# Optimization experiments

Measured on AMD Instinct MI355X. Metric: run time of the kernel, lower is better.

## Reference

```python
import jax, jax.numpy as jnp
import numpy as np

EPS = 1.0  # epsilon: defaults to 1.0 for scale-invariant kernels (thin_plate_spline)
TPS_MIN = 1e-7  # clamp in thin_plate_spline
NX, N, NDIM, M = 32768, 4096, 3, 16


def monomial_powers(ndim, degree):
    # replicates RBFBlock.monomial_powers for ndim=3, degree=1
    from itertools import combinations_with_replacement
    import math
    nmonos = math.comb(degree + ndim, ndim)
    out = np.zeros((nmonos, ndim), dtype=np.int32)
    count = 0
    for deg in range(degree + 1):
        for mono in combinations_with_replacement(range(ndim), deg):
            for var in mono:
                out[count, var] += 1
            count += 1
    return out


def setup_inputs() -> dict:
    key = jax.random.key(0)
    k1, k2, k3, k4 = jax.random.split(key, 4)
    powers = jnp.asarray(monomial_powers(NDIM, 1))  # (4, 3)
    return {
        "x": jax.random.normal(k1, (NX, NDIM), dtype=jnp.float32),
        "y": jax.random.normal(k2, (N, NDIM), dtype=jnp.float32),
        "shift": jax.random.normal(k3, (NDIM,), dtype=jnp.float32),
        "scale": jnp.ones((NDIM,), dtype=jnp.float32),
        "coeffs": jax.random.normal(k4, (N + powers.shape[0], M), dtype=jnp.float32) * 0.05,
        "powers": powers,
    }


def _cdist(a, b):
    # Euclidean distance matrix (na, nb) via the matmul identity; avoids (na, nb, d) blowup.
    a2 = jnp.sum(a * a, axis=1, keepdims=True)       # (na, 1)
    b2 = jnp.sum(b * b, axis=1, keepdims=True).T     # (1, nb)
    sq = a2 + b2 - 2.0 * (a @ b.T)
    return jnp.sqrt(jnp.maximum(sq, 0.0))


def _thin_plate_spline(r):
    r = jnp.maximum(r, TPS_MIN)
    return r * r * jnp.log(r)


def reference(x, y, shift, scale, coeffs, powers):
    # kernel part: phi(||eps*x - eps*y||)
    kv = _thin_plate_spline(_cdist(x * EPS, y * EPS))          # (nx, n)
    # polynomial part on normalized coords
    xhat = (x - shift) / scale                                  # (nx, d)
    p = jnp.prod(xhat[:, None, :] ** powers[None, :, :].astype(x.dtype), axis=-1)  # (nx, r)
    vec = jnp.concatenate([kv, p], axis=1)                      # (nx, n+r)
    return vec @ coeffs                                         # (nx, m)
```

## Files before the change

kernel.cpp:

```cpp
#include <hip/hip_runtime.h>

#define NXROWS 32768
#define NY     4096
#define MCOLS  16
#define BLOCK  256
#define KSPLIT 8
#define KCHUNK (NY / KSPLIT)
#define NITER  (KCHUNK / 32)
#define ROWS_PER_BLOCK 256
#define GRIDX  (NXROWS / ROWS_PER_BLOCK)

#define TPS_C 0.34657359027997264f

typedef __bf16 bf16x8 __attribute__((ext_vector_type(8)));
typedef short  s16x8  __attribute__((ext_vector_type(8)));
typedef float  f32x4  __attribute__((ext_vector_type(4)));

#define WS_Y4_OFF   0
#define WS_CT_OFF   65536
#define WS_PART_OFF 262144
#define WS_END      (WS_PART_OFF + (size_t)KSPLIT * NXROWS * MCOLS * 4)

static __device__ __forceinline__ unsigned short f2bfu(float f) {
    __bf16 h = (__bf16)f;
    return __builtin_bit_cast(unsigned short, h);
}

__global__ __launch_bounds__(BLOCK) void rbf_prep3(
    const float* __restrict__ y, const float* __restrict__ coeffs,
    float4* __restrict__ y4, unsigned int* __restrict__ cTw)
{
    const int idx = blockIdx.x * BLOCK + threadIdx.x;
    if (idx < MCOLS * NY / 2) {
        const int m  = idx >> 11;
        const int jp = (idx & 2047) * 2;
        const unsigned short u0 = f2bfu(TPS_C * coeffs[(size_t)jp * MCOLS + m]);
        const unsigned short u1 = f2bfu(TPS_C * coeffs[(size_t)(jp + 1) * MCOLS + m]);
        cTw[((size_t)m * NY + jp) >> 1] = (unsigned int)u0 | ((unsigned int)u1 << 16);
    } else {
        const int j = idx - MCOLS * NY / 2;
        const float y0 = y[3 * j], y1 = y[3 * j + 1], y2 = y[3 * j + 2];
        y4[j] = make_float4(y0, y1, y2, y0 * y0 + y1 * y1 + y2 * y2);
    }
}

__global__ __launch_bounds__(BLOCK, 4) void rbf_mfma4(
    const float* __restrict__ x, const float4* __restrict__ y4,
    const unsigned short* __restrict__ cT, float* __restrict__ part)
{
    const int lane = threadIdx.x & 63;
    const int wid  = threadIdx.x >> 6;
    const int n    = lane & 15;
    const int q    = lane >> 4;
    const int rowBase = blockIdx.x * ROWS_PER_BLOCK + wid * 64;
    const int kbase = blockIdx.y * KCHUNK;

    float sx[4], a0[4], a1[4], a2[4];
    #pragma unroll
    for (int t = 0; t < 4; ++t) {
        const int r = rowBase + t * 16 + n;
        const float c0 = x[r * 3], c1 = x[r * 3 + 1], c2 = x[r * 3 + 2];
        sx[t] = c0 * c0 + c1 * c1 + c2 * c2;
        a0[t] = -2.f * c0; a1[t] = -2.f * c1; a2[t] = -2.f * c2;
    }

    const float4* yb = y4 + kbase + q * 8;
    const unsigned short* cb = cT + (size_t)n * NY + kbase + q * 8;

    f32x4 acc[4];
    #pragma unroll
    for (int t = 0; t < 4; ++t) acc[t] = (f32x4){0.f, 0.f, 0.f, 0.f};

    for (int ks = 0; ks < NITER; ++ks) {
        float4 yv[8];
        #pragma unroll
        for (int e = 0; e < 8; ++e) yv[e] = yb[ks * 32 + e];
        const s16x8 braw = *reinterpret_cast<const s16x8*>(cb + ks * 32);

        bf16x8 af[4];
        #pragma unroll
        for (int e = 0; e < 8; ++e) {
            const float4 v = yv[e];
            #pragma unroll
            for (int t = 0; t < 4; ++t) {
                float s = fmaf(a0[t], v.x,
                          fmaf(a1[t], v.y,
                          fmaf(a2[t], v.z, sx[t] + v.w)));
                s = fmaxf(s, 1e-14f);
                af[t][e] = (__bf16)(s * __log2f(s));
            }
        }
        const bf16x8 bf = __builtin_bit_cast(bf16x8, braw);
        #pragma unroll
        for (int t = 0; t < 4; ++t)
            acc[t] = __builtin_amdgcn_mfma_f32_16x16x32_bf16(af[t], bf, acc[t], 0, 0, 0);
    }

    float* plane = part + (size_t)blockIdx.y * NXROWS * MCOLS;
    #pragma unroll
    for (int t = 0; t < 4; ++t) {
        float* o = plane + (size_t)(rowBase + t * 16 + q * 4) * MCOLS + n;
        #pragma unroll
        for (int r = 0; r < 4; ++r) o[(size_t)r * MCOLS] = acc[t][r];
    }
}

__global__ __launch_bounds__(BLOCK) void rbf_reduce(
    const float* __restrict__ part, const float* __restrict__ x,
    const float* __restrict__ shift, const float* __restrict__ scale,
    const float* __restrict__ coeffs, const int* __restrict__ powers,
    int nR, float* __restrict__ out)
{
    const int idx = blockIdx.x * BLOCK + threadIdx.x;
    const int row = idx >> 2, mq = idx & 3;
    f32x4 s = {0.f, 0.f, 0.f, 0.f};
    #pragma unroll
    for (int sp = 0; sp < KSPLIT; ++sp) {
        const f32x4 v = *reinterpret_cast<const f32x4*>(
            part + (size_t)sp * NXROWS * MCOLS + (size_t)row * MCOLS + mq * 4);
        s += v;
    }
    float xh[3];
    #pragma unroll
    for (int d = 0; d < 3; ++d) xh[d] = (x[row * 3 + d] - shift[d]) / scale[d];
    for (int r = 0; r < nR; ++r) {
        float p = 1.0f;
        for (int d = 0; d < 3; ++d) {
            const int pw = powers[r * 3 + d];
            for (int k = 0; k < pw; ++k) p *= xh[d];
        }
        const f32x4 cv = *reinterpret_cast<const f32x4*>(
            coeffs + (size_t)(NY + r) * MCOLS + mq * 4);
        s += p * cv;
    }
    *reinterpret_cast<f32x4*>(out + (size_t)row * MCOLS + mq * 4) = s;
}

__global__ __launch_bounds__(BLOCK) void rbf_f32_atomic(
    const float* __restrict__ x, const float* __restrict__ y,
    const float* __restrict__ coeffs, float* __restrict__ out)
{
    const int jbase = blockIdx.y * 512;
    const int row = blockIdx.x * BLOCK + threadIdx.x;
    const float x0 = x[row * 3], x1 = x[row * 3 + 1], x2 = x[row * 3 + 2];
    float acc[MCOLS];
    #pragma unroll
    for (int m = 0; m < MCOLS; ++m) acc[m] = 0.f;
    const float4* c4 = reinterpret_cast<const float4*>(coeffs) + (size_t)jbase * 4;
    for (int j = 0; j < 512; ++j) {
        const float dx = x0 - y[(jbase + j) * 3 + 0];
        const float dy = x1 - y[(jbase + j) * 3 + 1];
        const float dz = x2 - y[(jbase + j) * 3 + 2];
        const float sq = fmaxf(dx * dx + dy * dy + dz * dz, 1e-14f);
        const float t = TPS_C * sq * __log2f(sq);
        #pragma unroll
        for (int g = 0; g < 4; ++g) {
            const float4 cv = c4[j * 4 + g];
            acc[g * 4 + 0] += t * cv.x; acc[g * 4 + 1] += t * cv.y;
            acc[g * 4 + 2] += t * cv.z; acc[g * 4 + 3] += t * cv.w;
        }
    }
    #pragma unroll
    for (int m = 0; m < MCOLS; ++m)
        atomicAdd(&out[(size_t)row * MCOLS + m], acc[m]);
}

__global__ __launch_bounds__(BLOCK) void rbf_poly_atomic(
    const float* __restrict__ x, const float* __restrict__ shift,
    const float* __restrict__ scale, const float* __restrict__ coeffs,
    const int* __restrict__ powers, int nR, float* __restrict__ out)
{
    const int idx = blockIdx.x * BLOCK + threadIdx.x;
    const int row = idx >> 2, mq = idx & 3;
    float xh[3];
    #pragma unroll
    for (int d = 0; d < 3; ++d) xh[d] = (x[row * 3 + d] - shift[d]) / scale[d];
    f32x4 s = {0.f, 0.f, 0.f, 0.f};
    for (int r = 0; r < nR; ++r) {
        float p = 1.0f;
        for (int d = 0; d < 3; ++d) {
            const int pw = powers[r * 3 + d];
            for (int k = 0; k < pw; ++k) p *= xh[d];
        }
        const f32x4 cv = *reinterpret_cast<const f32x4*>(
            coeffs + (size_t)(NY + r) * MCOLS + mq * 4);
        s += p * cv;
    }
    float* o = out + (size_t)row * MCOLS + mq * 4;
    atomicAdd(o + 0, s.x); atomicAdd(o + 1, s.y);
    atomicAdd(o + 2, s.z); atomicAdd(o + 3, s.w);
}

extern "C" void kernel_launch(void* const* d_in, const int* in_sizes, int n_in,
                              void* d_out, int out_size, void* d_ws, size_t ws_size,
                              hipStream_t stream) {
    const float* x      = (const float*)d_in[0];
    const float* y      = (const float*)d_in[1];
    const float* shift  = (const float*)d_in[2];
    const float* scale  = (const float*)d_in[3];
    const float* coeffs = (const float*)d_in[4];
    const int*   powers = (const int*)d_in[5];
    const int    nR     = in_sizes[5] / 3;
    float* out = (float*)d_out;

    if (ws_size >= WS_END) {
        char* ws = (char*)d_ws;
        float4*         y4   = (float4*)(ws + WS_Y4_OFF);
        unsigned short* cT   = (unsigned short*)(ws + WS_CT_OFF);
        unsigned int*   cTw  = (unsigned int*)(ws + WS_CT_OFF);
        float*          part = (float*)(ws + WS_PART_OFF);
        rbf_prep3<<<(MCOLS * NY / 2 + NY) / BLOCK, BLOCK, 0, stream>>>(
            y, coeffs, y4, cTw);
        rbf_mfma4<<<dim3(GRIDX, KSPLIT), BLOCK, 0, stream>>>(x, y4, cT, part);
        rbf_reduce<<<NXROWS * 4 / BLOCK, BLOCK, 0, stream>>>(
            part, x, shift, scale, coeffs, powers, nR, out);
    } else {
        hipMemsetAsync(d_out, 0, (size_t)out_size * sizeof(float), stream);
        rbf_f32_atomic<<<dim3(NXROWS / BLOCK, NY / 512), BLOCK, 0, stream>>>(
            x, y, coeffs, out);
        rbf_poly_atomic<<<NXROWS * 4 / BLOCK, BLOCK, 0, stream>>>(
            x, shift, scale, coeffs, powers, nR, out);
    }
}
```

Measured before the change: 110.6 us.

## Stage y and coefficient chunks in LDS and double the K split

The MFMA kernel now loads its K-chunk of y (with the -2 factor folded into y during prep) and the bf16 coefficients into padded shared memory once per block, and reads from LDS inside the loop instead of global memory. KSPLIT goes from 8 to 16 so each block's chunk (256 entries) fits a single cooperative load, and occupancy is raised to 8 blocks per CU. The partial buffer and the reduce pass double in size, and each block now waits on a barrier after its load.

Result: slower. 118.5 us (+7.1%).

```diff
diff --git a/kernel.cpp b/kernel.cpp
--- a/kernel.cpp
+++ b/kernel.cpp
@@ -4,7 +4,7 @@
 #define NY     4096
 #define MCOLS  16
 #define BLOCK  256
-#define KSPLIT 8
+#define KSPLIT 16
 #define KCHUNK (NY / KSPLIT)
 #define NITER  (KCHUNK / 32)
 #define ROWS_PER_BLOCK 256
@@ -40,20 +40,38 @@
     } else {
         const int j = idx - MCOLS * NY / 2;
         const float y0 = y[3 * j], y1 = y[3 * j + 1], y2 = y[3 * j + 2];
-        y4[j] = make_float4(y0, y1, y2, y0 * y0 + y1 * y1 + y2 * y2);
-    }
-}
-
-__global__ __launch_bounds__(BLOCK, 4) void rbf_mfma4(
+        y4[j] = make_float4(-2.f * y0, -2.f * y1, -2.f * y2,
+                            y0 * y0 + y1 * y1 + y2 * y2);
+    }
+}
+
+__global__ __launch_bounds__(BLOCK, 8) void rbf_mfma5(
     const float* __restrict__ x, const float4* __restrict__ y4,
-    const unsigned short* __restrict__ cT, float* __restrict__ part)
-{
-    const int lane = threadIdx.x & 63;
-    const int wid  = threadIdx.x >> 6;
+    const unsigned int* __restrict__ cTw, float* __restrict__ part)
+{
+    __shared__ float4 ys[KCHUNK + KCHUNK / 8];
+    __shared__ unsigned short cs[MCOLS][KCHUNK + 8];
+
+    const int tid   = threadIdx.x;
+    const int kbase = blockIdx.y * KCHUNK;
+
+    ys[tid + (tid >> 3)] = y4[kbase + tid];
+    {
+        unsigned int* csw = reinterpret_cast<unsigned int*>(&cs[0][0]);
+        #pragma unroll
+        for (int i = tid; i < MCOLS * KCHUNK / 2; i += BLOCK) {
+            const int m = i >> 7;
+            const int c = i & 127;
+            csw[m * ((KCHUNK + 8) / 2) + c] = cTw[m * (NY / 2) + kbase / 2 + c];
+        }
+    }
+    __syncthreads();
+
+    const int lane = tid & 63;
+    const int wid  = tid >> 6;
     const int n    = lane & 15;
     const int q    = lane >> 4;
     const int rowBase = blockIdx.x * ROWS_PER_BLOCK + wid * 64;
-    const int kbase = blockIdx.y * KCHUNK;
 
     float sx[4], a0[4], a1[4], a2[4];
     #pragma unroll
@@ -61,26 +79,22 @@
         const int r = rowBase + t * 16 + n;
         const float c0 = x[r * 3], c1 = x[r * 3 + 1], c2 = x[r * 3 + 2];
         sx[t] = c0 * c0 + c1 * c1 + c2 * c2;
-        a0[t] = -2.f * c0; a1[t] = -2.f * c1; a2[t] = -2.f * c2;
-    }
-
-    const float4* yb = y4 + kbase + q * 8;
-    const unsigned short* cb = cT + (size_t)n * NY + kbase + q * 8;
+        a0[t] = c0; a1[t] = c1; a2[t] = c2;
+    }
+
+    const float4* ysp = ys + q * 9;
+    const unsigned short* csp = &cs[n][q * 8];
 
     f32x4 acc[4];
     #pragma unroll
     for (int t = 0; t < 4; ++t) acc[t] = (f32x4){0.f, 0.f, 0.f, 0.f};
 
     for (int ks = 0; ks < NITER; ++ks) {
-        float4 yv[8];
-        #pragma unroll
-        for (int e = 0; e < 8; ++e) yv[e] = yb[ks * 32 + e];
-        const s16x8 braw = *reinterpret_cast<const s16x8*>(cb + ks * 32);
-
+        const s16x8 braw = *reinterpret_cast<const s16x8*>(csp + ks * 32);
         bf16x8 af[4];
         #pragma unroll
         for (int e = 0; e < 8; ++e) {
-            const float4 v = yv[e];
+            const float4 v = ysp[ks * 36 + e];
             #pragma unroll
             for (int t = 0; t < 4; ++t) {
                 float s = fmaf(a0[t], v.x,
@@ -205,13 +219,12 @@
 
     if (ws_size >= WS_END) {
         char* ws = (char*)d_ws;
-        float4*         y4   = (float4*)(ws + WS_Y4_OFF);
-        unsigned short* cT   = (unsigned short*)(ws + WS_CT_OFF);
-        unsigned int*   cTw  = (unsigned int*)(ws + WS_CT_OFF);
-        float*          part = (float*)(ws + WS_PART_OFF);
+        float4*       y4   = (float4*)(ws + WS_Y4_OFF);
+        unsigned int* cTw  = (unsigned int*)(ws + WS_CT_OFF);
+        float*        part = (float*)(ws + WS_PART_OFF);
         rbf_prep3<<<(MCOLS * NY / 2 + NY) / BLOCK, BLOCK, 0, stream>>>(
             y, coeffs, y4, cTw);
-        rbf_mfma4<<<dim3(GRIDX, KSPLIT), BLOCK, 0, stream>>>(x, y4, cT, part);
+        rbf_mfma5<<<dim3(GRIDX, KSPLIT), BLOCK, 0, stream>>>(x, y4, cTw, part);
         rbf_reduce<<<NXROWS * 4 / BLOCK, BLOCK, 0, stream>>>(
             part, x, shift, scale, coeffs, powers, nR, out);
     } else {
```

## Compute squared distances with split-bf16 MFMA and permute into the coefficient MFMA

Applied to the files above, without the earlier changes.

The per-pair squared-distance FMAs are replaced by an MFMA. x and y are encoded as bf16 hi/lo splits so that a 16x16x32 bf16 MFMA yields |x|^2+|y|^2-2x·y in fp32. The distance tiles are then transformed by s*log2(s), packed to bf16, and rearranged across lanes with ds_bpermute into the A-operand layout for the existing coefficient MFMA. This moves most of the VALU distance arithmetic onto matrix cores, at the cost of extra MFMAs, cross-lane permutes, and some accuracy loss from the hi/lo bf16 splitting.

Result: slower. 116.3 us (+5.1%).

```diff
diff --git a/kernel.cpp b/kernel.cpp
--- a/kernel.cpp
+++ b/kernel.cpp
@@ -15,8 +15,9 @@
 typedef __bf16 bf16x8 __attribute__((ext_vector_type(8)));
 typedef short  s16x8  __attribute__((ext_vector_type(8)));
 typedef float  f32x4  __attribute__((ext_vector_type(4)));
-
-#define WS_Y4_OFF   0
+typedef unsigned int u32x4 __attribute__((ext_vector_type(4)));
+
+#define WS_Y8_OFF   0
 #define WS_CT_OFF   65536
 #define WS_PART_OFF 262144
 #define WS_END      (WS_PART_OFF + (size_t)KSPLIT * NXROWS * MCOLS * 4)
@@ -25,10 +26,13 @@
     __bf16 h = (__bf16)f;
     return __builtin_bit_cast(unsigned short, h);
 }
-
-__global__ __launch_bounds__(BLOCK) void rbf_prep3(
+static __device__ __forceinline__ unsigned int pku(float a, float b) {
+    return (unsigned int)f2bfu(a) | ((unsigned int)f2bfu(b) << 16);
+}
+
+__global__ __launch_bounds__(BLOCK) void rbf_prep4(
     const float* __restrict__ y, const float* __restrict__ coeffs,
-    float4* __restrict__ y4, unsigned int* __restrict__ cTw)
+    u32x4* __restrict__ y8, unsigned int* __restrict__ cTw)
 {
     const int idx = blockIdx.x * BLOCK + threadIdx.x;
     if (idx < MCOLS * NY / 2) {
@@ -40,31 +44,55 @@
     } else {
         const int j = idx - MCOLS * NY / 2;
         const float y0 = y[3 * j], y1 = y[3 * j + 1], y2 = y[3 * j + 2];
-        y4[j] = make_float4(y0, y1, y2, y0 * y0 + y1 * y1 + y2 * y2);
-    }
-}
-
-__global__ __launch_bounds__(BLOCK, 4) void rbf_mfma4(
-    const float* __restrict__ x, const float4* __restrict__ y4,
+        const float m0 = -2.f * y0, m1 = -2.f * y1, m2 = -2.f * y2;
+        const float s  = y0 * y0 + y1 * y1 + y2 * y2;
+        const float h0 = (float)(__bf16)m0, h1 = (float)(__bf16)m1, h2 = (float)(__bf16)m2;
+        const float sh = (float)(__bf16)s;
+        u32x4 v;
+        v.x = pku(h0, h1);
+        v.y = pku(h2, m0 - h0);
+        v.z = pku(m1 - h1, m2 - h2);
+        v.w = pku(s, s - sh);
+        y8[j] = v;
+    }
+}
+
+__global__ __launch_bounds__(BLOCK, 4) void rbf_mfma8(
+    const float* __restrict__ x, const u32x4* __restrict__ y8,
     const unsigned short* __restrict__ cT, float* __restrict__ part)
 {
     const int lane = threadIdx.x & 63;
     const int wid  = threadIdx.x >> 6;
     const int n    = lane & 15;
     const int q    = lane >> 4;
+    const bool q0  = (q == 0), q1 = (q == 1), q01 = (q < 2);
     const int rowBase = blockIdx.x * ROWS_PER_BLOCK + wid * 64;
     const int kbase = blockIdx.y * KCHUNK;
 
-    float sx[4], a0[4], a1[4], a2[4];
+    s16x8 bx[4];
     #pragma unroll
     for (int t = 0; t < 4; ++t) {
         const int r = rowBase + t * 16 + n;
-        const float c0 = x[r * 3], c1 = x[r * 3 + 1], c2 = x[r * 3 + 2];
-        sx[t] = c0 * c0 + c1 * c1 + c2 * c2;
-        a0[t] = -2.f * c0; a1[t] = -2.f * c1; a2[t] = -2.f * c2;
-    }
-
-    const float4* yb = y4 + kbase + q * 8;
+        const float x0 = x[r * 3], x1 = x[r * 3 + 1], x2 = x[r * 3 + 2];
+        const float s  = x0 * x0 + x1 * x1 + x2 * x2;
+        const float h0 = (float)(__bf16)x0, h1 = (float)(__bf16)x1, h2 = (float)(__bf16)x2;
+        const float sh = (float)(__bf16)s;
+        const unsigned int a0 = pku(h0, h1), a1 = pku(h2, h0), a2 = pku(h1, h2);
+        const unsigned int a3 = 0x3F803F80u;
+        const unsigned int b0 = pku(x0 - h0, x1 - h1);
+        const unsigned int b1 = pku(x2 - h2, s);
+        const unsigned int b2 = pku(s - sh, 0.f);
+        u32x4 w;
+        w.x = q0 ? a0 : (q1 ? b0 : 0u);
+        w.y = q0 ? a1 : (q1 ? b1 : 0u);
+        w.z = q0 ? a2 : (q1 ? b2 : 0u);
+        w.w = q0 ? a3 : 0u;
+        bx[t] = __builtin_bit_cast(s16x8, w);
+    }
+
+    const int ad1 = 4 * (n + 16 * ((2 * q) & 3));
+    const int ad2 = 4 * (n + 16 * ((2 * q + 1) & 3));
+
     const unsigned short* cb = cT + (size_t)n * NY + kbase + q * 8;
 
     f32x4 acc[4];
@@ -72,28 +100,60 @@
     for (int t = 0; t < 4; ++t) acc[t] = (f32x4){0.f, 0.f, 0.f, 0.f};
 
     for (int ks = 0; ks < NITER; ++ks) {
-        float4 yv[8];
+        const u32x4 Ylo = y8[kbase + ks * 32 + n];
+        const u32x4 Yhi = y8[kbase + ks * 32 + 16 + n];
+        const s16x8 bc  = *reinterpret_cast<const s16x8*>(cb + ks * 32);
+
+        u32x4 wa, wb;
+        wa.x = q01 ? Ylo.x : 0u;
+        wa.y = q0 ? Ylo.y : (q1 ? ((Ylo.y & 0xFFFFu) | 0x3F800000u) : 0u);
+        wa.z = q0 ? Ylo.z : (q1 ? 0x00003F80u : 0u);
+        wa.w = q0 ? Ylo.w : 0u;
+        wb.x = q01 ? Yhi.x : 0u;
+        wb.y = q0 ? Yhi.y : (q1 ? ((Yhi.y & 0xFFFFu) | 0x3F800000u) : 0u);
+        wb.z = q0 ? Yhi.z : (q1 ? 0x00003F80u : 0u);
+        wb.w = q0 ? Yhi.w : 0u;
+        const bf16x8 Alo = __builtin_bit_cast(bf16x8, wa);
+        const bf16x8 Ahi = __builtin_bit_cast(bf16x8, wb);
+        const bf16x8 bcf = __builtin_bit_cast(bf16x8, bc);
+
         #pragma unroll
-        for (int e = 0; e < 8; ++e) yv[e] = yb[ks * 32 + e];
-        const s16x8 braw = *reinterpret_cast<const s16x8*>(cb + ks * 32);
-
-        bf16x8 af[4];
-        #pragma unroll
-        for (int e = 0; e < 8; ++e) {
-            const float4 v = yv[e];
+        for (int t = 0; t < 4; ++t) {
+            const bf16x8 bxt = __builtin_bit_cast(bf16x8, bx[t]);
+            f32x4 Dlo = __builtin_amdgcn_mfma_f32_16x16x32_bf16(
+                Alo, bxt, (f32x4){0.f, 0.f, 0.f, 0.f}, 0, 0, 0);
+            f32x4 Dhi = __builtin_amdgcn_mfma_f32_16x16x32_bf16(
+                Ahi, bxt, (f32x4){0.f, 0.f, 0.f, 0.f}, 0, 0, 0);
+            float tl[4], th[4];
             #pragma unroll
-            for (int t = 0; t < 4; ++t) {
-                float s = fmaf(a0[t], v.x,
-                          fmaf(a1[t], v.y,
-                          fmaf(a2[t], v.z, sx[t] + v.w)));
-                s = fmaxf(s, 1e-14f);
-                af[t][e] = (__bf16)(s * __log2f(s));
+            for (int r = 0; r < 4; ++r) {
+                float sl = fmaxf(Dlo[r], 1e-14f);
+                float sh = fmaxf(Dhi[r], 1e-14f);
+                tl[r] = sl * __log2f(sl);
+                th[r] = sh * __log2f(sh);
             }
-        }
-        const bf16x8 bf = __builtin_bit_cast(bf16x8, braw);
-        #pragma unroll
-        for (int t = 0; t < 4; ++t)
-            acc[t] = __builtin_amdgcn_mfma_f32_16x16x32_bf16(af[t], bf, acc[t], 0, 0, 0);
+            const int ul0 = (int)pku(tl[0], tl[1]);
+            const int ul1 = (int)pku(tl[2], tl[3]);
+            const int uh0 = (int)pku(th[0], th[1]);
+            const int uh1 = (int)pku(th[2], th[3]);
+            u32x4 wp;
+            {
+                const int l0 = __builtin_amdgcn_ds_bpermute(ad1, ul0);
+                const int h0 = __builtin_amdgcn_ds_bpermute(ad1, uh0);
+                const int l1 = __builtin_amdgcn_ds_bpermute(ad1, ul1);
+                const int h1 = __builtin_amdgcn_ds_bpermute(ad1, uh1);
+                const int l2 = __builtin_amdgcn_ds_bpermute(ad2, ul0);
+                const int h2 = __builtin_amdgcn_ds_bpermute(ad2, uh0);
+                const int l3 = __builtin_amdgcn_ds_bpermute(ad2, ul1);
+                const int h3 = __builtin_amdgcn_ds_bpermute(ad2, uh1);
+                wp.x = (unsigned int)(q01 ? l0 : h0);
+                wp.y = (unsigned int)(q01 ? l1 : h1);
+                wp.z = (unsigned int)(q01 ? l2 : h2);
+                wp.w = (unsigned int)(q01 ? l3 : h3);
+            }
+            const bf16x8 A2 = __builtin_bit_cast(bf16x8, wp);
+            acc[t] = __builtin_amdgcn_mfma_f32_16x16x32_bf16(A2, bcf, acc[t], 0, 0, 0);
+        }
     }
 
     float* plane = part + (size_t)blockIdx.y * NXROWS * MCOLS;
@@ -205,13 +265,13 @@
 
     if (ws_size >= WS_END) {
         char* ws = (char*)d_ws;
-        float4*         y4   = (float4*)(ws + WS_Y4_OFF);
+        u32x4*          y8   = (u32x4*)(ws + WS_Y8_OFF);
         unsigned short* cT   = (unsigned short*)(ws + WS_CT_OFF);
         unsigned int*   cTw  = (unsigned int*)(ws + WS_CT_OFF);
         float*          part = (float*)(ws + WS_PART_OFF);
-        rbf_prep3<<<(MCOLS * NY / 2 + NY) / BLOCK, BLOCK, 0, stream>>>(
-            y, coeffs, y4, cTw);
-        rbf_mfma4<<<dim3(GRIDX, KSPLIT), BLOCK, 0, stream>>>(x, y4, cT, part);
+        rbf_prep4<<<(MCOLS * NY / 2 + NY) / BLOCK, BLOCK, 0, stream>>>(
+            y, coeffs, y8, cTw);
+        rbf_mfma8<<<dim3(GRIDX, KSPLIT), BLOCK, 0, stream>>>(x, y8, cT, part);
         rbf_reduce<<<NXROWS * 4 / BLOCK, BLOCK, 0, stream>>>(
             part, x, shift, scale, coeffs, powers, nR, out);
     } else {
```
